# Kernel tuning notes

Hardware: AMD Instinct MI355X
Metric: run time of the kernel (lower is better)

The kernel has to match this reference:

```python
import jax, jax.numpy as jnp
import numpy as np

B = 16384
STATE = 524   # state_dim / output_size
IENC = 256    # INet output dim
ZD = 32       # z_dim
H = 256       # expert hidden size
E = 5         # num_experts
HG = 256      # gating hidden size
IN1 = STATE + IENC + ZD   # 812, PredictionNet layer-1 input
IN2 = H + ZD              # 288, layers 2/3 input


def _uni(k, shape):
    # matches PredictionNet.init_params glorot-style uniform bound
    bound = float(np.sqrt(6.0 / (shape[-2] * shape[-1])))
    return jax.random.uniform(k, shape, jnp.float32, -bound, bound)


def setup_inputs() -> dict:
    key = jax.random.key(0)
    ks = jax.random.split(key, 12)
    d = {}
    d['z'] = jax.random.normal(ks[0], (B, ZD), jnp.float32)
    d['p_prev'] = jax.random.normal(ks[1], (B, STATE), jnp.float32)
    d['I'] = jax.random.normal(ks[2], (B, 2048), jnp.float32)
    # gating network: (state+z) -> HG -> HG//2 -> E
    d['gw1'] = _uni(ks[3], (STATE + ZD, HG)); d['gb1'] = jnp.zeros((HG,), jnp.float32)
    d['gw2'] = _uni(ks[4], (HG, HG // 2));    d['gb2'] = jnp.zeros((HG // 2,), jnp.float32)
    d['gw3'] = _uni(ks[5], (HG // 2, E));     d['gb3'] = jnp.zeros((E,), jnp.float32)
    # INet: 2048 -> 256 -> 256 -> 256
    d['iw1'] = _uni(ks[6], (2048, IENC)); d['ib1'] = jnp.zeros((IENC,), jnp.float32)
    d['iw2'] = _uni(ks[7], (IENC, IENC)); d['ib2'] = jnp.zeros((IENC,), jnp.float32)
    d['iw3'] = _uni(ks[8], (IENC, IENC)); d['ib3'] = jnp.zeros((IENC,), jnp.float32)
    # expert weights [E, in, out], biases [E, out]
    d['w_l1'] = _uni(ks[9], (E, IN1, H));     d['b_l1'] = jnp.zeros((E, H), jnp.float32)
    d['w_l2'] = _uni(ks[10], (E, IN2, H));    d['b_l2'] = jnp.zeros((E, H), jnp.float32)
    d['w_l3'] = _uni(ks[11], (E, IN2, STATE)); d['b_l3'] = jnp.zeros((E, STATE), jnp.float32)
    return d


def reference(z, p_prev, I, gw1, gb1, gw2, gb2, gw3, gb3,
              iw1, ib1, iw2, ib2, iw3, ib3,
              w_l1, b_l1, w_l2, b_l2, w_l3, b_l3):
    elu = jax.nn.elu
    # gating network -> softmax blending coefficients omega [B, E]
    g = elu(jnp.concatenate([z, p_prev], axis=1) @ gw1 + gb1)
    g = elu(g @ gw2 + gb2)
    omega = jax.nn.softmax(g @ gw3 + gb3, axis=-1)
    # interaction encoder
    Ienc = elu(elu(elu(I @ iw1 + ib1) @ iw2 + ib2) @ iw3 + ib3)
    x = jnp.concatenate([p_prev, Ienc], axis=1)  # [B, STATE+IENC]

    def moe_linear(h, W, b):
        # same math as sum_e omega_e * (h @ W_e) + omega @ b, without
        # materializing per-sample blended [B, in, out] weights
        per_expert = jnp.einsum('bi,eio->beo', h, W)
        return jnp.einsum('be,beo->bo', omega, per_expert) + omega @ b

    h0 = jnp.concatenate([z, x], axis=1)          # [B, 812]
    h1 = elu(moe_linear(h0, w_l1, b_l1))          # [B, 256]
    h2 = elu(moe_linear(jnp.concatenate([z, h1], axis=1), w_l2, b_l2))
    h3 = moe_linear(jnp.concatenate([z, h2], axis=1), w_l3, b_l3)  # [B, 524]
    return h3
```

## Files before the change

### kernel.cpp

```cpp
#include <hip/hip_runtime.h>
#include <hip/hip_bf16.h>
#include <cstdint>
#include <cstddef>


#define BATCH 16384

typedef __attribute__((ext_vector_type(8))) short short8;
typedef __attribute__((ext_vector_type(4))) float f32x4;
typedef unsigned short u16;
typedef unsigned int u32;

__device__ __forceinline__ float bf2f(u16 u) {
  union { float f; u32 i; } v; v.i = ((u32)u) << 16; return v.f;
}
__device__ __forceinline__ u16 f2bf(float f) {
  union { float f; u32 i; } v; v.f = f;
  u32 x = v.i;
  return (u16)((x + 0x7fffu + ((x >> 16) & 1u)) >> 16);
}
__device__ __forceinline__ u16 load_bf(const void* p, long i, int f32) {
  return f32 ? f2bf(((const float*)p)[i]) : ((const u16*)p)[i];
}
__device__ __forceinline__ float elu_f(float x) { return x > 0.f ? x : expm1f(x); }

__global__ __launch_bounds__(256) void detect_dtype(const u32* __restrict__ zr,
                                                    int* __restrict__ flag)
{
  __shared__ int cnt;
  if (threadIdx.x == 0) cnt = 0;
  __syncthreads();
  u32 w = zr[threadIdx.x];
  int e = (w >> 7) & 0xFF;
  if (e >= 112 && e <= 142) atomicAdd(&cnt, 1);
  __syncthreads();
  if (threadIdx.x == 0) *flag = (cnt < 128) ? 1 : 0;
}

__global__ __launch_bounds__(256) void prep_kernel(
    const void* __restrict__ z, const void* __restrict__ p,
    const int* __restrict__ flagp,
    u16* __restrict__ h0, u16* __restrict__ h1c, u16* __restrict__ h2c,
    const void* ib1, const void* ib2, const void* ib3,
    const void* gb1, const void* gb2, const void* gb3,
    const void* gw3, const void* bl1, const void* bl2, const void* bl3,
    u16* __restrict__ smallc)
{
  const int f32 = *flagp;
  const long gid0 = (long)blockIdx.x * blockDim.x + threadIdx.x;
  if (gid0 < 7100) {
    long j = gid0; u16 v;
    if      (j < 256)  v = load_bf(ib1, j,        f32);
    else if (j < 512)  v = load_bf(ib2, j - 256,  f32);
    else if (j < 768)  v = load_bf(ib3, j - 512,  f32);
    else if (j < 1024) v = load_bf(gb1, j - 768,  f32);
    else if (j < 1152) v = load_bf(gb2, j - 1024, f32);
    else if (j < 1280) v = (j - 1152 < 5) ? load_bf(gb3, j - 1152, f32) : (u16)0;
    else if (j < 1920) v = load_bf(gw3, j - 1280, f32);
    else if (j < 3200) v = load_bf(bl1, j - 1920, f32);
    else if (j < 4480) v = load_bf(bl2, j - 3200, f32);
    else               v = load_bf(bl3, j - 4480, f32);
    smallc[j] = v;
  }
  const long total = (long)BATCH * 832;
  const long stride = (long)gridDim.x * blockDim.x;
  for (long i = gid0; i < total; i += stride) {
    int b = (int)(i / 832);
    int c = (int)(i - (long)b * 832);
    if (c < 32) {
      u16 v = load_bf(z, (long)b * 32 + c, f32);
      h0[i] = v;
      h1c[(long)b * 288 + c] = v;
      h2c[(long)b * 288 + c] = v;
    } else if (c < 556) {
      h0[i] = load_bf(p, (long)b * 524 + (c - 32), f32);
    } else if (c >= 812) {
      h0[i] = 0;
    }
  }
}

__global__ __launch_bounds__(256) void convert_I(
    const void* __restrict__ I, const int* __restrict__ flagp,
    u16* __restrict__ out)
{
  const int f32 = *flagp;
  const long total8 = (long)BATCH * 2048 / 8;
  const long stride = (long)gridDim.x * blockDim.x;
  for (long t = (long)blockIdx.x * blockDim.x + threadIdx.x; t < total8; t += stride) {
    if (f32) {
      const float4* src = (const float4*)I;
      float4 a = src[t * 2], b = src[t * 2 + 1];
      union { u16 r[8]; uint4 v; } u;
      u.r[0] = f2bf(a.x); u.r[1] = f2bf(a.y); u.r[2] = f2bf(a.z); u.r[3] = f2bf(a.w);
      u.r[4] = f2bf(b.x); u.r[5] = f2bf(b.y); u.r[6] = f2bf(b.z); u.r[7] = f2bf(b.w);
      *(uint4*)(out + t * 8) = u.v;
    } else {
      *(uint4*)(out + t * 8) = ((const uint4*)I)[t];
    }
  }
}

__global__ __launch_bounds__(256) void transpose_pad(
    const void* __restrict__ in, const int* __restrict__ flagp,
    u16* __restrict__ out, int E, int K, int N, int Kp, int Np)
{
  const int f32 = *flagp;
  const long total = (long)E * Np * Kp;
  const long stride = (long)gridDim.x * blockDim.x;
  for (long i = (long)blockIdx.x * blockDim.x + threadIdx.x; i < total; i += stride) {
    int k = (int)(i % Kp);
    long t = i / Kp;
    int n = (int)(t % Np);
    int e = (int)(t / Np);
    u16 v = 0;
    if (k < K && n < N) v = load_bf(in, (long)e * K * N + (long)k * N + n, f32);
    out[i] = v;
  }
}

template<bool ELU>
__global__ __launch_bounds__(256) void gemm128(
    const u16* __restrict__ A, int lda,
    const u16* __restrict__ Wt, int ldw,
    const u16* __restrict__ bias,
    u16* __restrict__ C, int ldc, int col_off, int K)
{
  constexpr int LDSK = 40;
  __shared__ __align__(16) u16 sA[128 * LDSK];
  __shared__ __align__(16) u16 sB[128 * LDSK];

  const int tid  = threadIdx.x;
  const int bm   = blockIdx.x, bn = blockIdx.y;
  const int lane = tid & 63, wave = tid >> 6;
  const int wm = (wave & 1) * 64, wn = (wave >> 1) * 64;
  const int lrow = lane & 15, lq = lane >> 4;

  const int srow = tid >> 2;
  const int schunk = (tid & 3) * 8;

  const u16* Ag = A  + (size_t)(bm * 128) * lda;
  const u16* Wg = Wt + (size_t)(bn * 128) * ldw;

  f32x4 acc[4][4] = {};

  for (int k0 = 0; k0 < K; k0 += 32) {
    __syncthreads();
    {
      uint4 a0 = *(const uint4*)(Ag + (size_t)srow * lda + k0 + schunk);
      uint4 a1 = *(const uint4*)(Ag + (size_t)(srow + 64) * lda + k0 + schunk);
      uint4 b0 = *(const uint4*)(Wg + (size_t)srow * ldw + k0 + schunk);
      uint4 b1 = *(const uint4*)(Wg + (size_t)(srow + 64) * ldw + k0 + schunk);
      *(uint4*)(sA + srow * LDSK + schunk) = a0;
      *(uint4*)(sA + (srow + 64) * LDSK + schunk) = a1;
      *(uint4*)(sB + srow * LDSK + schunk) = b0;
      *(uint4*)(sB + (srow + 64) * LDSK + schunk) = b1;
    }
    __syncthreads();

    short8 a[4], b[4];
#pragma unroll
    for (int i = 0; i < 4; ++i)
      a[i] = *(const short8*)(sA + (wm + i * 16 + lrow) * LDSK + lq * 8);
#pragma unroll
    for (int i = 0; i < 4; ++i)
      b[i] = *(const short8*)(sB + (wn + i * 16 + lrow) * LDSK + lq * 8);

#pragma unroll
    for (int mi = 0; mi < 4; ++mi)
#pragma unroll
      for (int ni = 0; ni < 4; ++ni)
        acc[mi][ni] = __builtin_amdgcn_mfma_f32_16x16x32_bf16(a[mi], b[ni], acc[mi][ni], 0, 0, 0);
  }

#pragma unroll
  for (int ni = 0; ni < 4; ++ni) {
    const int col = bn * 128 + wn + ni * 16 + lrow;
    const float bv = bf2f(bias[col]);
#pragma unroll
    for (int mi = 0; mi < 4; ++mi) {
#pragma unroll
      for (int r = 0; r < 4; ++r) {
        const int row = bm * 128 + wm + mi * 16 + lq * 4 + r;
        float v = acc[mi][ni][r] + bv;
        if (ELU) v = elu_f(v);
        C[(size_t)row * ldc + col_off + col] = f2bf(v);
      }
    }
  }
}

__global__ __launch_bounds__(256) void gating3_kernel(
    const u16* __restrict__ g2, const u16* __restrict__ gw3c,
    const u16* __restrict__ gb3c, float* __restrict__ omega)
{
  const int wid  = (blockIdx.x << 2) + (threadIdx.x >> 6);
  const int lane = threadIdx.x & 63;
  const u32 gp = *(const u32*)(g2 + (size_t)wid * 128 + lane * 2);
  const float x0 = bf2f((u16)(gp & 0xffffu));
  const float x1 = bf2f((u16)(gp >> 16));
  float acc[5];
#pragma unroll
  for (int e = 0; e < 5; ++e)
    acc[e] = x0 * bf2f(gw3c[(lane * 2) * 5 + e]) + x1 * bf2f(gw3c[(lane * 2 + 1) * 5 + e]);
#pragma unroll
  for (int off = 1; off < 64; off <<= 1) {
#pragma unroll
    for (int e = 0; e < 5; ++e) acc[e] += __shfl_xor(acc[e], off);
  }
  if (lane == 0) {
    float t[5], m = -1e30f;
#pragma unroll
    for (int e = 0; e < 5; ++e) { t[e] = acc[e] + bf2f(gb3c[e]); m = fmaxf(m, t[e]); }
    float s = 0.f;
#pragma unroll
    for (int e = 0; e < 5; ++e) { t[e] = expf(t[e] - m); s += t[e]; }
    const float inv = 1.f / s;
#pragma unroll
    for (int e = 0; e < 5; ++e) omega[(size_t)wid * 5 + e] = t[e] * inv;
  }
}

template<bool ELU>
__global__ __launch_bounds__(256) void moe_gemm(
    const u16* __restrict__ A, int lda,
    const u16* __restrict__ Wt, int ldw, long wstride_e,
    const u16* __restrict__ bias, int bias_n,
    const float* __restrict__ omega,
    void* __restrict__ C, int ldc, int col_off, int n_store, int K,
    const int* __restrict__ flagp, int is_final)
{
  constexpr int LDSK = 40;
  __shared__ __align__(16) u16 sA[64 * LDSK];
  __shared__ __align__(16) u16 sW[5][64 * LDSK];
  __shared__ float som[64 * 5];
  __shared__ float sbias[5][64];

  const int tid  = threadIdx.x;
  const int bm   = blockIdx.x, bn = blockIdx.y;
  const int lane = tid & 63, wave = tid >> 6;
  const int wm = (wave & 1) * 32, wn = (wave >> 1) * 32;
  const int lrow = lane & 15, lq = lane >> 4;
  const int f32out = is_final ? *flagp : 0;

  for (int t = tid; t < 320; t += 256) {
    som[t] = omega[(size_t)(bm * 64) * 5 + t];
    const int e = t >> 6, c = t & 63;
    const int col = bn * 64 + c;
    sbias[e][c] = (col < bias_n) ? bf2f(bias[(size_t)e * bias_n + col]) : 0.f;
  }

  const int srow = tid >> 2;
  const int schunk = (tid & 3) * 8;

  const u16* Ag = A  + (size_t)(bm * 64) * lda;
  const u16* Wg = Wt + (size_t)(bn * 64) * ldw;

  f32x4 acc[5][2][2] = {};

  for (int k0 = 0; k0 < K; k0 += 32) {
    __syncthreads();
    *(uint4*)(sA + srow * LDSK + schunk) =
        *(const uint4*)(Ag + (size_t)srow * lda + k0 + schunk);
#pragma unroll
    for (int e = 0; e < 5; ++e)
      *(uint4*)(sW[e] + srow * LDSK + schunk) =
          *(const uint4*)(Wg + e * wstride_e + (size_t)srow * ldw + k0 + schunk);
    __syncthreads();

    short8 a0 = *(const short8*)(sA + (wm + lrow) * LDSK + lq * 8);
    short8 a1 = *(const short8*)(sA + (wm + 16 + lrow) * LDSK + lq * 8);
#pragma unroll
    for (int e = 0; e < 5; ++e) {
      short8 b0 = *(const short8*)(sW[e] + (wn + lrow) * LDSK + lq * 8);
      short8 b1 = *(const short8*)(sW[e] + (wn + 16 + lrow) * LDSK + lq * 8);
      acc[e][0][0] = __builtin_amdgcn_mfma_f32_16x16x32_bf16(a0, b0, acc[e][0][0], 0, 0, 0);
      acc[e][0][1] = __builtin_amdgcn_mfma_f32_16x16x32_bf16(a0, b1, acc[e][0][1], 0, 0, 0);
      acc[e][1][0] = __builtin_amdgcn_mfma_f32_16x16x32_bf16(a1, b0, acc[e][1][0], 0, 0, 0);
      acc[e][1][1] = __builtin_amdgcn_mfma_f32_16x16x32_bf16(a1, b1, acc[e][1][1], 0, 0, 0);
    }
  }

#pragma unroll
  for (int mi = 0; mi < 2; ++mi) {
#pragma unroll
    for (int r = 0; r < 4; ++r) {
      const int rl = wm + mi * 16 + lq * 4 + r;
      const int row = bm * 64 + rl;
      float om[5];
#pragma unroll
      for (int e = 0; e < 5; ++e) om[e] = som[rl * 5 + e];
#pragma unroll
      for (int ni = 0; ni < 2; ++ni) {
        const int c = wn + ni * 16 + lrow;
        const int col = bn * 64 + c;
        if (col < n_store) {
          float v = 0.f;
#pragma unroll
          for (int e = 0; e < 5; ++e) v += om[e] * (acc[e][mi][ni][r] + sbias[e][c]);
          if (ELU) v = elu_f(v);
          const size_t idx = (size_t)row * ldc + col_off + col;
          if (f32out) ((float*)C)[idx] = v;
          else        ((u16*)C)[idx]   = f2bf(v);
        }
      }
    }
  }
}

static inline int tblocks(long total) {
  long b = (total + 255) / 256;
  return (int)(b < 2048 ? b : 2048);
}

extern "C" void kernel_launch(void* const* d_in, const int* in_sizes, int n_in,
                              void* d_out, int out_size, void* d_ws, size_t ws_size,
                              hipStream_t stream)
{
  const void* z    = d_in[0];
  const void* pprev= d_in[1];
  const void* I    = d_in[2];
  const void* gw1  = d_in[3];
  const void* gb1  = d_in[4];
  const void* gw2  = d_in[5];
  const void* gb2  = d_in[6];
  const void* gw3  = d_in[7];
  const void* gb3  = d_in[8];
  const void* iw1  = d_in[9];
  const void* ib1  = d_in[10];
  const void* ib2  = d_in[12];
  const void* iw2  = d_in[11];
  const void* iw3  = d_in[13];
  const void* ib3  = d_in[14];
  const void* wl1  = d_in[15];
  const void* bl1  = d_in[16];
  const void* wl2  = d_in[17];
  const void* bl2  = d_in[18];
  const void* wl3  = d_in[19];
  const void* bl3  = d_in[20];

  char* base = (char*)d_ws;
  size_t off = 0;
  auto alloc = [&](size_t bytes) -> void* {
    void* p = base + off;
    off = (off + bytes + 255) & ~(size_t)255;
    return p;
  };

  const size_t B = BATCH;
  int* flagp   = (int*)alloc(256);
  u16* h0      = (u16*)alloc(B * 832 * 2);
  u16* h1c     = (u16*)alloc(B * 288 * 2);
  u16* h2c     = (u16*)alloc(B * 288 * 2);
  u16* i1      = (u16*)alloc(B * 256 * 2);
  u16* i2      = (u16*)alloc(B * 256 * 2);
  float* omega = (float*)alloc(B * 5 * 4);
  u16* Ibf     = (u16*)alloc(B * 2048 * 2);
  u16* smallc  = (u16*)alloc(7100 * 2);
  u16* iw1t = (u16*)alloc((size_t)256 * 2048 * 2);
  u16* iw2t = (u16*)alloc((size_t)256 * 256 * 2);
  u16* iw3t = (u16*)alloc((size_t)256 * 256 * 2);
  u16* gw1t = (u16*)alloc((size_t)256 * 576 * 2);
  u16* gw2t = (u16*)alloc((size_t)128 * 256 * 2);
  u16* wl1t = (u16*)alloc((size_t)5 * 256 * 832 * 2);
  u16* wl2t = (u16*)alloc((size_t)5 * 256 * 288 * 2);
  u16* wl3t = (u16*)alloc((size_t)5 * 576 * 288 * 2);
  u16* g1 = i1;
  u16* g2 = i2;
  (void)in_sizes; (void)n_in; (void)out_size; (void)ws_size;

  u16* ib1c = smallc + 0,   *ib2c = smallc + 256, *ib3c = smallc + 512;
  u16* gb1c = smallc + 768, *gb2c = smallc + 1024, *gb3c = smallc + 1152;
  u16* gw3c = smallc + 1280;
  u16* bl1c = smallc + 1920, *bl2c = smallc + 3200, *bl3c = smallc + 4480;

  detect_dtype<<<1, 256, 0, stream>>>((const u32*)z, flagp);
  prep_kernel<<<4096, 256, 0, stream>>>(z, pprev, flagp, h0, h1c, h2c,
      ib1, ib2, ib3, gb1, gb2, gb3, gw3, bl1, bl2, bl3, smallc);
  convert_I<<<4096, 256, 0, stream>>>(I, flagp, Ibf);
  transpose_pad<<<tblocks((long)1*256*2048), 256, 0, stream>>>(iw1, flagp, iw1t, 1, 2048, 256, 2048, 256);
  transpose_pad<<<tblocks((long)1*256*256),  256, 0, stream>>>(iw2, flagp, iw2t, 1, 256, 256, 256, 256);
  transpose_pad<<<tblocks((long)1*256*256),  256, 0, stream>>>(iw3, flagp, iw3t, 1, 256, 256, 256, 256);
  transpose_pad<<<tblocks((long)1*256*576),  256, 0, stream>>>(gw1, flagp, gw1t, 1, 556, 256, 576, 256);
  transpose_pad<<<tblocks((long)1*128*256),  256, 0, stream>>>(gw2, flagp, gw2t, 1, 256, 128, 256, 128);
  transpose_pad<<<tblocks((long)5*256*832),  256, 0, stream>>>(wl1, flagp, wl1t, 5, 812, 256, 832, 256);
  transpose_pad<<<tblocks((long)5*256*288),  256, 0, stream>>>(wl2, flagp, wl2t, 5, 288, 256, 288, 256);
  transpose_pad<<<tblocks((long)5*576*288),  256, 0, stream>>>(wl3, flagp, wl3t, 5, 288, 524, 288, 576);

  gemm128<true><<<dim3(BATCH/128, 2), 256, 0, stream>>>(Ibf, 2048, iw1t, 2048, ib1c, i1, 256, 0,   2048);
  gemm128<true><<<dim3(BATCH/128, 2), 256, 0, stream>>>(i1,  256,  iw2t, 256,  ib2c, i2, 256, 0,   256);
  gemm128<true><<<dim3(BATCH/128, 2), 256, 0, stream>>>(i2,  256,  iw3t, 256,  ib3c, h0, 832, 556, 256);

  gemm128<true><<<dim3(BATCH/128, 2), 256, 0, stream>>>(h0, 832, gw1t, 576, gb1c, g1, 256, 0, 576);
  gemm128<true><<<dim3(BATCH/128, 1), 256, 0, stream>>>(g1, 256, gw2t, 256, gb2c, g2, 128, 0, 256);
  gating3_kernel<<<BATCH/4, 256, 0, stream>>>(g2, gw3c, gb3c, omega);

  moe_gemm<true><<<dim3(BATCH/64, 4), 256, 0, stream>>>(
      h0, 832, wl1t, 832, (long)256 * 832, bl1c, 256, omega, h1c, 288, 32, 256, 832, flagp, 0);
  moe_gemm<true><<<dim3(BATCH/64, 4), 256, 0, stream>>>(
      h1c, 288, wl2t, 288, (long)256 * 288, bl2c, 256, omega, h2c, 288, 32, 256, 288, flagp, 0);
  moe_gemm<false><<<dim3(BATCH/64, 9), 256, 0, stream>>>(
      h2c, 288, wl3t, 288, (long)576 * 288, bl3c, 524, omega, d_out, 524, 0, 524, 288, flagp, 1);
}
```

Baseline: 630.7 us.

## Use direct global-to-LDS loads with XOR swizzle and merge transpose launches

Both GEMM kernels now stage tiles through global_load_lds (direct-to-LDS) with an XOR swizzle in place of padded LDS rows. This removes the register round-trip on loads and avoids bank conflicts. The eight transpose_pad launches are merged into a single transpose_all kernel that walks a segment table, and prep_kernel now uses a 2D grid with one row per block instead of a grid-stride loop with div/mod. The swizzle is applied on the source side of the load, which needs the wave-to-LDS mapping to line up exactly, and there is no double buffering, so load latency is still exposed at each barrier.

Result: no change. 642.4 us (+1.9%).

```diff
diff --git a/kernel.cpp b/kernel.cpp
--- a/kernel.cpp
+++ b/kernel.cpp
@@ -11,6 +11,13 @@
 typedef unsigned short u16;
 typedef unsigned int u32;
 
+typedef __attribute__((address_space(3))) void lds_t;
+typedef __attribute__((address_space(1))) void gmem_t;
+
+__device__ __forceinline__ void gload16(const u16* g, u16* l) {
+  __builtin_amdgcn_global_load_lds((gmem_t*)(u16*)g, (lds_t*)l, 16, 0, 0);
+}
+
 __device__ __forceinline__ float bf2f(u16 u) {
   union { float f; u32 i; } v; v.i = ((u32)u) << 16; return v.f;
 }
@@ -23,6 +30,8 @@
   return f32 ? f2bf(((const float*)p)[i]) : ((const u16*)p)[i];
 }
 __device__ __forceinline__ float elu_f(float x) { return x > 0.f ? x : expm1f(x); }
+
+__device__ __forceinline__ int swz(int row, int q) { return q ^ ((row >> 1) & 3); }
 
 __global__ __launch_bounds__(256) void detect_dtype(const u32* __restrict__ zr,
                                                     int* __restrict__ flag)
@@ -47,36 +56,35 @@
     u16* __restrict__ smallc)
 {
   const int f32 = *flagp;
-  const long gid0 = (long)blockIdx.x * blockDim.x + threadIdx.x;
-  if (gid0 < 7100) {
-    long j = gid0; u16 v;
-    if      (j < 256)  v = load_bf(ib1, j,        f32);
-    else if (j < 512)  v = load_bf(ib2, j - 256,  f32);
-    else if (j < 768)  v = load_bf(ib3, j - 512,  f32);
-    else if (j < 1024) v = load_bf(gb1, j - 768,  f32);
-    else if (j < 1152) v = load_bf(gb2, j - 1024, f32);
-    else if (j < 1280) v = (j - 1152 < 5) ? load_bf(gb3, j - 1152, f32) : (u16)0;
-    else if (j < 1920) v = load_bf(gw3, j - 1280, f32);
-    else if (j < 3200) v = load_bf(bl1, j - 1920, f32);
-    else if (j < 4480) v = load_bf(bl2, j - 3200, f32);
-    else               v = load_bf(bl3, j - 4480, f32);
-    smallc[j] = v;
-  }
-  const long total = (long)BATCH * 832;
-  const long stride = (long)gridDim.x * blockDim.x;
-  for (long i = gid0; i < total; i += stride) {
-    int b = (int)(i / 832);
-    int c = (int)(i - (long)b * 832);
-    if (c < 32) {
-      u16 v = load_bf(z, (long)b * 32 + c, f32);
-      h0[i] = v;
-      h1c[(long)b * 288 + c] = v;
-      h2c[(long)b * 288 + c] = v;
-    } else if (c < 556) {
-      h0[i] = load_bf(p, (long)b * 524 + (c - 32), f32);
-    } else if (c >= 812) {
-      h0[i] = 0;
-    }
+  const int b = blockIdx.y;
+  const int c = blockIdx.x * 256 + threadIdx.x;
+  if (blockIdx.y == 0 && blockIdx.x == 0) {
+    for (long j = threadIdx.x; j < 7100; j += 256) {
+      u16 v;
+      if      (j < 256)  v = load_bf(ib1, j,        f32);
+      else if (j < 512)  v = load_bf(ib2, j - 256,  f32);
+      else if (j < 768)  v = load_bf(ib3, j - 512,  f32);
+      else if (j < 1024) v = load_bf(gb1, j - 768,  f32);
+      else if (j < 1152) v = load_bf(gb2, j - 1024, f32);
+      else if (j < 1280) v = (j - 1152 < 5) ? load_bf(gb3, j - 1152, f32) : (u16)0;
+      else if (j < 1920) v = load_bf(gw3, j - 1280, f32);
+      else if (j < 3200) v = load_bf(bl1, j - 1920, f32);
+      else if (j < 4480) v = load_bf(bl2, j - 3200, f32);
+      else               v = load_bf(bl3, j - 4480, f32);
+      smallc[j] = v;
+    }
+  }
+  if (c >= 832) return;
+  const long i = (long)b * 832 + c;
+  if (c < 32) {
+    u16 v = load_bf(z, (long)b * 32 + c, f32);
+    h0[i] = v;
+    h1c[(long)b * 288 + c] = v;
+    h2c[(long)b * 288 + c] = v;
+  } else if (c < 556) {
+    h0[i] = load_bf(p, (long)b * 524 + (c - 32), f32);
+  } else if (c >= 812) {
+    h0[i] = 0;
   }
 }
 
@@ -101,21 +109,42 @@
   }
 }
 
-__global__ __launch_bounds__(256) void transpose_pad(
-    const void* __restrict__ in, const int* __restrict__ flagp,
-    u16* __restrict__ out, int E, int K, int N, int Kp, int Np)
-{
+struct TPSeg { long end; int K, N, Kp, Np; };
+
+__global__ __launch_bounds__(256) void transpose_all(
+    const int* __restrict__ flagp,
+    const void* s0, const void* s1, const void* s2, const void* s3,
+    const void* s4, const void* s5, const void* s6, const void* s7,
+    u16* d0, u16* d1, u16* d2, u16* d3, u16* d4, u16* d5, u16* d6, u16* d7)
+{
+  const TPSeg seg[8] = {
+    {  524288, 2048, 256, 2048, 256 },
+    {  589824,  256, 256,  256, 256 },
+    {  655360,  256, 256,  256, 256 },
+    {  802816,  556, 256,  576, 256 },
+    {  835584,  256, 128,  256, 128 },
+    { 1900544,  812, 256,  832, 256 },
+    { 2269184,  288, 256,  288, 256 },
+    { 3098624,  288, 524,  288, 576 },
+  };
+  const void* const srcs[8] = { s0, s1, s2, s3, s4, s5, s6, s7 };
+  u16* const dsts[8] = { d0, d1, d2, d3, d4, d5, d6, d7 };
   const int f32 = *flagp;
-  const long total = (long)E * Np * Kp;
+  const long total = 3098624;
   const long stride = (long)gridDim.x * blockDim.x;
   for (long i = (long)blockIdx.x * blockDim.x + threadIdx.x; i < total; i += stride) {
-    int k = (int)(i % Kp);
-    long t = i / Kp;
-    int n = (int)(t % Np);
-    int e = (int)(t / Np);
+    int s = 0;
+    long base = 0;
+    while (i >= seg[s].end) { base = seg[s].end; ++s; }
+    const long j = i - base;
+    const int Kp = seg[s].Kp, Np = seg[s].Np, K = seg[s].K, N = seg[s].N;
+    const int k = (int)(j % Kp);
+    const long t = j / Kp;
+    const int n = (int)(t % Np);
+    const int e = (int)(t / Np);
     u16 v = 0;
-    if (k < K && n < N) v = load_bf(in, (long)e * K * N + (long)k * N + n, f32);
-    out[i] = v;
+    if (k < K && n < N) v = load_bf(srcs[s], (long)e * K * N + (long)k * N + n, f32);
+    dsts[s][j] = v;
   }
 }
 
@@ -126,9 +155,8 @@
     const u16* __restrict__ bias,
     u16* __restrict__ C, int ldc, int col_off, int K)
 {
-  constexpr int LDSK = 40;
-  __shared__ __align__(16) u16 sA[128 * LDSK];
-  __shared__ __align__(16) u16 sB[128 * LDSK];
+  __shared__ __align__(16) u16 sA[128 * 32];
+  __shared__ __align__(16) u16 sB[128 * 32];
 
   const int tid  = threadIdx.x;
   const int bm   = blockIdx.x, bn = blockIdx.y;
@@ -136,35 +164,34 @@
   const int wm = (wave & 1) * 64, wn = (wave >> 1) * 64;
   const int lrow = lane & 15, lq = lane >> 4;
 
-  const int srow = tid >> 2;
-  const int schunk = (tid & 3) * 8;
-
-  const u16* Ag = A  + (size_t)(bm * 128) * lda;
-  const u16* Wg = Wt + (size_t)(bn * 128) * ldw;
+  const int srow0 = 32 * wave + (lane >> 2);
+  const int sq    = (lane & 3) ^ ((lane >> 3) & 3);
+  const u16* Ag = A  + (size_t)(bm * 128 + srow0) * lda + sq * 8;
+  const u16* Wg = Wt + (size_t)(bn * 128 + srow0) * ldw + sq * 8;
+  u16* lA = sA + wave * 1024;
+  u16* lB = sB + wave * 1024;
 
   f32x4 acc[4][4] = {};
 
   for (int k0 = 0; k0 < K; k0 += 32) {
     __syncthreads();
-    {
-      uint4 a0 = *(const uint4*)(Ag + (size_t)srow * lda + k0 + schunk);
-      uint4 a1 = *(const uint4*)(Ag + (size_t)(srow + 64) * lda + k0 + schunk);
-      uint4 b0 = *(const uint4*)(Wg + (size_t)srow * ldw + k0 + schunk);
-      uint4 b1 = *(const uint4*)(Wg + (size_t)(srow + 64) * ldw + k0 + schunk);
-      *(uint4*)(sA + srow * LDSK + schunk) = a0;
-      *(uint4*)(sA + (srow + 64) * LDSK + schunk) = a1;
-      *(uint4*)(sB + srow * LDSK + schunk) = b0;
-      *(uint4*)(sB + (srow + 64) * LDSK + schunk) = b1;
-    }
+    gload16(Ag + k0, lA);
+    gload16(Ag + (size_t)16 * lda + k0, lA + 512);
+    gload16(Wg + k0, lB);
+    gload16(Wg + (size_t)16 * ldw + k0, lB + 512);
     __syncthreads();
 
     short8 a[4], b[4];
 #pragma unroll
-    for (int i = 0; i < 4; ++i)
-      a[i] = *(const short8*)(sA + (wm + i * 16 + lrow) * LDSK + lq * 8);
-#pragma unroll
-    for (int i = 0; i < 4; ++i)
-      b[i] = *(const short8*)(sB + (wn + i * 16 + lrow) * LDSK + lq * 8);
+    for (int i = 0; i < 4; ++i) {
+      const int r = wm + i * 16 + lrow;
+      a[i] = *(const short8*)(sA + r * 32 + swz(r, lq) * 8);
+    }
+#pragma unroll
+    for (int i = 0; i < 4; ++i) {
+      const int r = wn + i * 16 + lrow;
+      b[i] = *(const short8*)(sB + r * 32 + swz(r, lq) * 8);
+    }
 
 #pragma unroll
     for (int mi = 0; mi < 4; ++mi)
@@ -230,9 +257,8 @@
     void* __restrict__ C, int ldc, int col_off, int n_store, int K,
     const int* __restrict__ flagp, int is_final)
 {
-  constexpr int LDSK = 40;
-  __shared__ __align__(16) u16 sA[64 * LDSK];
-  __shared__ __align__(16) u16 sW[5][64 * LDSK];
+  __shared__ __align__(16) u16 sA[64 * 32];
+  __shared__ __align__(16) u16 sW[5][64 * 32];
   __shared__ float som[64 * 5];
   __shared__ float sbias[5][64];
 
@@ -250,30 +276,33 @@
     sbias[e][c] = (col < bias_n) ? bf2f(bias[(size_t)e * bias_n + col]) : 0.f;
   }
 
-  const int srow = tid >> 2;
-  const int schunk = (tid & 3) * 8;
-
-  const u16* Ag = A  + (size_t)(bm * 64) * lda;
-  const u16* Wg = Wt + (size_t)(bn * 64) * ldw;
+  const int srow = 16 * wave + (lane >> 2);
+  const int sq   = (lane & 3) ^ ((lane >> 3) & 3);
+  const u16* Ag = A  + (size_t)(bm * 64 + srow) * lda + sq * 8;
+  const u16* Wg = Wt + (size_t)(bn * 64 + srow) * ldw + sq * 8;
+  u16* lA = sA + wave * 512;
+  const int lWoff = wave * 512;
 
   f32x4 acc[5][2][2] = {};
 
   for (int k0 = 0; k0 < K; k0 += 32) {
     __syncthreads();
-    *(uint4*)(sA + srow * LDSK + schunk) =
-        *(const uint4*)(Ag + (size_t)srow * lda + k0 + schunk);
+    gload16(Ag + k0, lA);
 #pragma unroll
     for (int e = 0; e < 5; ++e)
-      *(uint4*)(sW[e] + srow * LDSK + schunk) =
-          *(const uint4*)(Wg + e * wstride_e + (size_t)srow * ldw + k0 + schunk);
+      gload16(Wg + e * wstride_e + k0, sW[e] + lWoff);
     __syncthreads();
 
-    short8 a0 = *(const short8*)(sA + (wm + lrow) * LDSK + lq * 8);
-    short8 a1 = *(const short8*)(sA + (wm + 16 + lrow) * LDSK + lq * 8);
+    const int ra0 = wm + lrow, ra1 = ra0 + 16;
+    short8 a0 = *(const short8*)(sA + ra0 * 32 + swz(ra0, lq) * 8);
+    short8 a1 = *(const short8*)(sA + ra1 * 32 + swz(ra1, lq) * 8);
+    const int rb0 = wn + lrow, rb1 = rb0 + 16;
+    const int ob0 = rb0 * 32 + swz(rb0, lq) * 8;
+    const int ob1 = rb1 * 32 + swz(rb1, lq) * 8;
 #pragma unroll
     for (int e = 0; e < 5; ++e) {
-      short8 b0 = *(const short8*)(sW[e] + (wn + lrow) * LDSK + lq * 8);
-      short8 b1 = *(const short8*)(sW[e] + (wn + 16 + lrow) * LDSK + lq * 8);
+      short8 b0 = *(const short8*)(sW[e] + ob0);
+      short8 b1 = *(const short8*)(sW[e] + ob1);
       acc[e][0][0] = __builtin_amdgcn_mfma_f32_16x16x32_bf16(a0, b0, acc[e][0][0], 0, 0, 0);
       acc[e][0][1] = __builtin_amdgcn_mfma_f32_16x16x32_bf16(a0, b1, acc[e][0][1], 0, 0, 0);
       acc[e][1][0] = __builtin_amdgcn_mfma_f32_16x16x32_bf16(a1, b0, acc[e][1][0], 0, 0, 0);
@@ -306,11 +335,6 @@
       }
     }
   }
-}
-
-static inline int tblocks(long total) {
-  long b = (total + 255) / 256;
-  return (int)(b < 2048 ? b : 2048);
 }
 
 extern "C" void kernel_launch(void* const* d_in, const int* in_sizes, int n_in,
@@ -328,8 +352,8 @@
   const void* gb3  = d_in[8];
   const void* iw1  = d_in[9];
   const void* ib1  = d_in[10];
+  const void* iw2  = d_in[11];
   const void* ib2  = d_in[12];
-  const void* iw2  = d_in[11];
   const void* iw3  = d_in[13];
   const void* ib3  = d_in[14];
   const void* wl1  = d_in[15];
@@ -375,17 +399,12 @@
   u16* bl1c = smallc + 1920, *bl2c = smallc + 3200, *bl3c = smallc + 4480;
 
   detect_dtype<<<1, 256, 0, stream>>>((const u32*)z, flagp);
-  prep_kernel<<<4096, 256, 0, stream>>>(z, pprev, flagp, h0, h1c, h2c,
+  prep_kernel<<<dim3(4, BATCH), 256, 0, stream>>>(z, pprev, flagp, h0, h1c, h2c,
       ib1, ib2, ib3, gb1, gb2, gb3, gw3, bl1, bl2, bl3, smallc);
   convert_I<<<4096, 256, 0, stream>>>(I, flagp, Ibf);
-  transpose_pad<<<tblocks((long)1*256*2048), 256, 0, stream>>>(iw1, flagp, iw1t, 1, 2048, 256, 2048, 256);
-  transpose_pad<<<tblocks((long)1*256*256),  256, 0, stream>>>(iw2, flagp, iw2t, 1, 256, 256, 256, 256);
-  transpose_pad<<<tblocks((long)1*256*256),  256, 0, stream>>>(iw3, flagp, iw3t, 1, 256, 256, 256, 256);
-  transpose_pad<<<tblocks((long)1*256*576),  256, 0, stream>>>(gw1, flagp, gw1t, 1, 556, 256, 576, 256);
-  transpose_pad<<<tblocks((long)1*128*256),  256, 0, stream>>>(gw2, flagp, gw2t, 1, 256, 128, 256, 128);
-  transpose_pad<<<tblocks((long)5*256*832),  256, 0, stream>>>(wl1, flagp, wl1t, 5, 812, 256, 832, 256);
-  transpose_pad<<<tblocks((long)5*256*288),  256, 0, stream>>>(wl2, flagp, wl2t, 5, 288, 256, 288, 256);
-  transpose_pad<<<tblocks((long)5*576*288),  256, 0, stream>>>(wl3, flagp, wl3t, 5, 288, 524, 288, 576);
+  transpose_all<<<3072, 256, 0, stream>>>(flagp,
+      iw1, iw2, iw3, gw1, gw2, wl1, wl2, wl3,
+      iw1t, iw2t, iw3t, gw1t, gw2t, wl1t, wl2t, wl3t);
 
   gemm128<true><<<dim3(BATCH/128, 2), 256, 0, stream>>>(Ibf, 2048, iw1t, 2048, ib1c, i1, 256, 0,   2048);
   gemm128<true><<<dim3(BATCH/128, 2), 256, 0, stream>>>(i1,  256,  iw2t, 256,  ib2c, i2, 256, 0,   256);
```
